# Kernel optimization log

Hardware: AMD Instinct MI355X
Metric: run time of the kernel (lower is better)

## Reference

```python
import jax, jax.numpy as jnp
import numpy as np

N_NODES = 100000


def _gcn_norm(edge_index, num_nodes):
    """Replicates remove_self_loops + add_self_loops + symmetric deg norm.

    Instead of dynamically removing/appending edges (data-dependent shapes),
    we mask out self-loop edges and handle the added self loops analytically:
    each node gets exactly one self loop with value deg_inv_sqrt[i]**2.
    """
    row, col = edge_index[0], edge_index[1]
    not_self = (row != col).astype(jnp.float32)  # mask removed self loops
    # degree(row) after removing self loops and adding one self loop per node
    deg = jax.ops.segment_sum(not_self, row, num_segments=num_nodes) + 1.0
    deg_inv_sqrt = jnp.where(deg > 0, jax.lax.rsqrt(deg), 0.0)
    edge_norm = deg_inv_sqrt[row] * deg_inv_sqrt[col] * not_self  # [E]
    self_norm = deg_inv_sqrt * deg_inv_sqrt  # [N] diagonal of normalized adj
    return row, col, edge_norm, self_norm


def _spmm(row, col, edge_norm, self_norm, h):
    # y = A_norm @ h, with A_norm = off-diagonal edges + diagonal self loops
    msgs = edge_norm[:, None] * h[col]  # [E, F] gather + scale
    y = jax.ops.segment_sum(msgs, row, num_segments=h.shape[0])
    return y + self_norm[:, None] * h


def setup_inputs() -> dict:
    key = jax.random.key(0)
    k1, k2, k3 = jax.random.split(key, 3)
    E = 3200000
    edge_index = jax.random.randint(k1, (2, E), 0, N_NODES, dtype=jnp.int32)
    x = jax.random.normal(k2, (N_NODES, 128), dtype=jnp.float32)
    W = jax.random.normal(k3, (128, 64), dtype=jnp.float32)
    return {"edge_index": edge_index, "x": x, "W": W}


def reference(edge_index, x, W):
    num_nodes = x.shape[0]
    row, col, edge_norm, self_norm = _gcn_norm(edge_index, num_nodes)
    h = x @ W  # [N, out]
    # matmul(A@A, h) == A @ (A @ h): avoid materializing sparse A^2
    h = _spmm(row, col, edge_norm, self_norm, h)
    h = _spmm(row, col, edge_norm, self_norm, h)
    return h
```

## Files before the change

### kernel.cpp

```cpp
#include <hip/hip_runtime.h>
#include <hip/hip_fp16.h>


#define RPB 1024
#define RPB_SHIFT 10
#define CBITS 17
#define CMASK ((1 << CBITS) - 1)
#define P1_TPB 1024
#define P1_EPT 8
#define P1_CHUNK (P1_TPB * P1_EPT)
#define MAXNB 128
#define BCAP 36864

typedef _Float16 f16x8 __attribute__((ext_vector_type(8)));
typedef float f32x4 __attribute__((ext_vector_type(4)));

__global__ __launch_bounds__(128) void k_init_bcur(int* __restrict__ bcur, int nb) {
  int b = blockIdx.x * 128 + threadIdx.x;
  if (b < nb) bcur[b] = b * BCAP;
}

__global__ __launch_bounds__(P1_TPB) void k_part1(const int* __restrict__ rows,
                                                  const int* __restrict__ cols,
                                                  int* __restrict__ bcur,
                                                  int* __restrict__ pairs,
                                                  int E, int nb) {
  __shared__ int hist[MAXNB];
  __shared__ int goff[MAXNB];
  int tid = threadIdx.x;
  long base = (long)blockIdx.x * P1_CHUNK;
  int r[P1_EPT], c[P1_EPT];
#pragma unroll
  for (int i = 0; i < P1_EPT; ++i) {
    long e = base + (long)i * P1_TPB + tid;
    if (e < E) {
      r[i] = rows[e];
      c[i] = cols[e];
    } else {
      r[i] = -1;
      c[i] = -1;
    }
  }
  if (tid < nb) hist[tid] = 0;
  __syncthreads();
#pragma unroll
  for (int i = 0; i < P1_EPT; ++i)
    if (r[i] != c[i]) atomicAdd(&hist[r[i] >> RPB_SHIFT], 1);
  __syncthreads();
  if (tid < nb) {
    int h = hist[tid];
    goff[tid] = h ? atomicAdd(&bcur[tid], h) : 0;
    hist[tid] = 0;
  }
  __syncthreads();
#pragma unroll
  for (int i = 0; i < P1_EPT; ++i) {
    if (r[i] != c[i]) {
      int b = r[i] >> RPB_SHIFT;
      int rank = atomicAdd(&hist[b], 1);
      pairs[goff[b] + rank] = ((r[i] & (RPB - 1)) << CBITS) | c[i];
    }
  }
}

__global__ __launch_bounds__(P1_TPB) void k_part3(const int* __restrict__ bcur,
                                                  const int* __restrict__ pairs,
                                                  int* __restrict__ colidx,
                                                  int* __restrict__ row_start,
                                                  int* __restrict__ deg,
                                                  float* __restrict__ dis,
                                                  float* __restrict__ selfn, int n) {
  __shared__ int lh[RPB];
  __shared__ int lscan[RPB];
  int tid = threadIdx.x;
  int b = blockIdx.x;
  int base = b * RPB;
  int e0 = b * BCAP;
  int e1 = bcur[b];
  lh[tid] = 0;
  __syncthreads();
  for (int i = e0 + tid; i < e1; i += P1_TPB)
    atomicAdd(&lh[pairs[i] >> CBITS], 1);
  __syncthreads();
  int d = lh[tid];
  int row = base + tid;
  if (row < n) {
    float dd = (float)d + 1.0f;
    dis[row] = rsqrtf(dd);
    selfn[row] = 1.0f / dd;
    deg[row] = d;
  }
  lscan[tid] = d;
  __syncthreads();
  for (int off = 1; off < RPB; off <<= 1) {
    int t = (tid >= off) ? lscan[tid - off] : 0;
    __syncthreads();
    lscan[tid] += t;
    __syncthreads();
  }
  int rstart = e0 + lscan[tid] - d;
  if (row < n) row_start[row] = rstart;
  lh[tid] = rstart;
  __syncthreads();
  for (int i = e0 + tid; i < e1; i += P1_TPB) {
    int v = pairs[i];
    int p = atomicAdd(&lh[v >> CBITS], 1);
    colidx[p] = v & CMASK;
  }
}

#define XPAD 136
__global__ __launch_bounds__(256) void k_gemm_mfma(const float* __restrict__ x,
                                                   const float* __restrict__ W,
                                                   const float* __restrict__ dis,
                                                   __half* __restrict__ g, int n) {
  __shared__ _Float16 xs[64 * XPAD];
  __shared__ _Float16 wt[64 * XPAD];
  int tid = threadIdx.x;
  int row0 = blockIdx.x * 64;
  for (int i = 0; i < 32; ++i) {
    int idx = tid + i * 256;
    int k = idx >> 6, f = idx & 63;
    wt[f * XPAD + k] = (_Float16)W[idx];
  }
  {
    int lrow = tid >> 2;
    int kb = (tid & 3) * 32;
    int row = row0 + lrow;
    _Float16* dst = &xs[lrow * XPAD + kb];
    if (row < n) {
      const float* src = x + (size_t)row * 128 + kb;
#pragma unroll
      for (int jj = 0; jj < 4; ++jj) {
        float4 v0 = *(const float4*)(src + jj * 8);
        float4 v1 = *(const float4*)(src + jj * 8 + 4);
        f16x8 t;
        t[0] = (_Float16)v0.x; t[1] = (_Float16)v0.y;
        t[2] = (_Float16)v0.z; t[3] = (_Float16)v0.w;
        t[4] = (_Float16)v1.x; t[5] = (_Float16)v1.y;
        t[6] = (_Float16)v1.z; t[7] = (_Float16)v1.w;
        *(f16x8*)(dst + jj * 8) = t;
      }
    } else {
      f16x8 z = {};
#pragma unroll
      for (int jj = 0; jj < 4; ++jj) *(f16x8*)(dst + jj * 8) = z;
    }
  }
  __syncthreads();
  int wid = tid >> 6, lane = tid & 63;
  int lr = lane & 15;
  int lk = (lane >> 4) * 8;
  f32x4 acc[4] = {{0.f, 0.f, 0.f, 0.f}, {0.f, 0.f, 0.f, 0.f},
                  {0.f, 0.f, 0.f, 0.f}, {0.f, 0.f, 0.f, 0.f}};
  const _Float16* xbase = &xs[(wid * 16 + lr) * XPAD + lk];
  const _Float16* wbase = &wt[lr * XPAD + lk];
#pragma unroll
  for (int ks = 0; ks < 4; ++ks) {
    f16x8 a = *(const f16x8*)(xbase + ks * 32);
#pragma unroll
    for (int ft = 0; ft < 4; ++ft) {
      f16x8 b = *(const f16x8*)(wbase + (size_t)ft * 16 * XPAD + ks * 32);
      acc[ft] = __builtin_amdgcn_mfma_f32_16x16x32_f16(a, b, acc[ft], 0, 0, 0);
    }
  }
  int mrow = row0 + wid * 16 + (lane >> 4) * 4;
#pragma unroll
  for (int j = 0; j < 4; ++j) {
    int row = mrow + j;
    if (row < n) {
      float dsc = dis[row];
#pragma unroll
      for (int ft = 0; ft < 4; ++ft)
        g[(size_t)row * 64 + ft * 16 + lr] = __float2half_rn(dsc * acc[ft][j]);
    }
  }
}

template <bool OUTF32>
__global__ __launch_bounds__(256) void k_spmm_h(const int* __restrict__ row_start,
                                                const int* __restrict__ deg,
                                                const int* __restrict__ colidx,
                                                const float* __restrict__ scale,
                                                const __half* __restrict__ gin,
                                                void* __restrict__ gout, int n) {
  int lane = threadIdx.x & 63;
  int wid = threadIdx.x >> 6;
  int r = blockIdx.x * 8 + wid * 2 + (lane >> 5);
  if (r >= n) return;
  int f2 = lane & 31;
  const __half2* gin2 = (const __half2*)gin;
  int start = row_start[r];
  int len = deg[r];
  float2 sv = __half22float2(gin2[(size_t)r * 32 + f2]);
  float ax = sv.x, ay = sv.y;
  int j = 0;
  for (; j + 16 <= len; j += 16) {
    int c[16];
#pragma unroll
    for (int u = 0; u < 16; ++u) c[u] = colidx[start + j + u];
    float2 v[16];
#pragma unroll
    for (int u = 0; u < 16; ++u) v[u] = __half22float2(gin2[(size_t)c[u] * 32 + f2]);
#pragma unroll
    for (int u = 0; u < 16; ++u) {
      ax += v[u].x;
      ay += v[u].y;
    }
  }
  for (; j + 4 <= len; j += 4) {
    int c0 = colidx[start + j + 0];
    int c1 = colidx[start + j + 1];
    int c2 = colidx[start + j + 2];
    int c3 = colidx[start + j + 3];
    float2 v0 = __half22float2(gin2[(size_t)c0 * 32 + f2]);
    float2 v1 = __half22float2(gin2[(size_t)c1 * 32 + f2]);
    float2 v2 = __half22float2(gin2[(size_t)c2 * 32 + f2]);
    float2 v3 = __half22float2(gin2[(size_t)c3 * 32 + f2]);
    ax += v0.x + v1.x + v2.x + v3.x;
    ay += v0.y + v1.y + v2.y + v3.y;
  }
  for (; j < len; ++j) {
    int c = colidx[start + j];
    float2 v = __half22float2(gin2[(size_t)c * 32 + f2]);
    ax += v.x;
    ay += v.y;
  }
  float s = scale[r];
  if (OUTF32) {
    ((float2*)gout)[(size_t)r * 32 + f2] = make_float2(s * ax, s * ay);
  } else {
    ((__half2*)gout)[(size_t)r * 32 + f2] = __floats2half2_rn(s * ax, s * ay);
  }
}

extern "C" void kernel_launch(void* const* d_in, const int* in_sizes, int n_in,
                              void* d_out, int out_size, void* d_ws, size_t ws_size,
                              hipStream_t stream) {
  const int* edge = (const int*)d_in[0];
  const float* x = (const float*)d_in[1];
  const float* W = (const float*)d_in[2];
  float* out = (float*)d_out;

  int E = in_sizes[0] / 2;
  int N = in_sizes[1] / 128;
  const int* rows = edge;
  const int* cols = edge + E;
  int nbuckets = (N + RPB - 1) / RPB;

  char* p = (char*)d_ws;
  auto alloc = [&](size_t bytes) {
    char* q = p;
    p += (bytes + 255) & ~(size_t)255;
    return q;
  };
  size_t slots = (size_t)nbuckets * BCAP;
  int* deg       = (int*)alloc((size_t)N * 4);
  int* row_start = (int*)alloc((size_t)N * 4);
  int* bcur      = (int*)alloc((size_t)nbuckets * 4);
  int* colidx    = (int*)alloc(slots * 4);
  float* dis     = (float*)alloc((size_t)N * 4);
  float* selfn   = (float*)alloc((size_t)N * 4);
  __half* g      = (__half*)alloc((size_t)N * 64 * 2);
  size_t g1_bytes = (size_t)N * 64 * 2;
  size_t pairs_bytes = slots * 4;
  char* g1_raw = (char*)alloc(g1_bytes > pairs_bytes ? g1_bytes : pairs_bytes);
  __half* g1 = (__half*)g1_raw;
  int* pairs = (int*)g1_raw;

  int p1_blocks = (int)(((long)E + P1_CHUNK - 1) / P1_CHUNK);

  k_init_bcur<<<(nbuckets + 127) / 128, 128, 0, stream>>>(bcur, nbuckets);
  k_part1<<<p1_blocks, P1_TPB, 0, stream>>>(rows, cols, bcur, pairs, E, nbuckets);
  k_part3<<<nbuckets, P1_TPB, 0, stream>>>(bcur, pairs, colidx, row_start, deg,
                                           dis, selfn, N);

  k_gemm_mfma<<<(N + 63) / 64, 256, 0, stream>>>(x, W, dis, g, N);

  k_spmm_h<false><<<(N + 7) / 8, 256, 0, stream>>>(row_start, deg, colidx, selfn,
                                                   g, (void*)g1, N);

  k_spmm_h<true><<<(N + 7) / 8, 256, 0, stream>>>(row_start, deg, colidx, dis,
                                                  g1, (void*)out, N);
}
```

Before: 194.7 us.

## Split feature dimension into 16-wide slices to shrink SpMM gather working set

The GEMM now writes the fp16 features in a sliced layout of four slices, each [N,16]. Each SpMM pass is split into four launches that process one 16-feature slice, so the gathered table per launch is N*32 bytes and fits better in cache, with 8 lanes per row instead of 32. Column-index loads and output stores are marked nontemporal so they do not evict the gather table. The cost is reading colidx four times per pass, issuing eight SpMM launches instead of two, and doing 32-byte gathers per neighbor.

```diff
diff --git a/kernel.cpp b/kernel.cpp
--- a/kernel.cpp
+++ b/kernel.cpp
@@ -14,6 +14,7 @@
 
 typedef _Float16 f16x8 __attribute__((ext_vector_type(8)));
 typedef float f32x4 __attribute__((ext_vector_type(4)));
+typedef float f32x2 __attribute__((ext_vector_type(2)));
 
 __global__ __launch_bounds__(128) void k_init_bcur(int* __restrict__ bcur, int nb) {
   int b = blockIdx.x * 128 + threadIdx.x;
@@ -172,36 +173,39 @@
       float dsc = dis[row];
 #pragma unroll
       for (int ft = 0; ft < 4; ++ft)
-        g[(size_t)row * 64 + ft * 16 + lr] = __float2half_rn(dsc * acc[ft][j]);
+        g[((size_t)ft * n + row) * 16 + lr] = __float2half_rn(dsc * acc[ft][j]);
     }
   }
 }
 
 template <bool OUTF32>
-__global__ __launch_bounds__(256) void k_spmm_h(const int* __restrict__ row_start,
+__global__ __launch_bounds__(256) void k_spmm_s(const int* __restrict__ row_start,
                                                 const int* __restrict__ deg,
                                                 const int* __restrict__ colidx,
                                                 const float* __restrict__ scale,
-                                                const __half* __restrict__ gin,
-                                                void* __restrict__ gout, int n) {
-  int lane = threadIdx.x & 63;
-  int wid = threadIdx.x >> 6;
-  int r = blockIdx.x * 8 + wid * 2 + (lane >> 5);
+                                                const __half2* __restrict__ gslice,
+                                                void* __restrict__ gout,
+                                                int n, int fbase) {
+  int tid = threadIdx.x;
+  int lane = tid & 63;
+  int wid = tid >> 6;
+  int rslot = lane >> 3;
+  int f2 = lane & 7;
+  int r = blockIdx.x * 32 + wid * 8 + rslot;
   if (r >= n) return;
-  int f2 = lane & 31;
-  const __half2* gin2 = (const __half2*)gin;
   int start = row_start[r];
   int len = deg[r];
-  float2 sv = __half22float2(gin2[(size_t)r * 32 + f2]);
+  float2 sv = __half22float2(gslice[r * 8 + f2]);
   float ax = sv.x, ay = sv.y;
   int j = 0;
   for (; j + 16 <= len; j += 16) {
     int c[16];
 #pragma unroll
-    for (int u = 0; u < 16; ++u) c[u] = colidx[start + j + u];
+    for (int u = 0; u < 16; ++u)
+      c[u] = __builtin_nontemporal_load(&colidx[start + j + u]);
     float2 v[16];
 #pragma unroll
-    for (int u = 0; u < 16; ++u) v[u] = __half22float2(gin2[(size_t)c[u] * 32 + f2]);
+    for (int u = 0; u < 16; ++u) v[u] = __half22float2(gslice[c[u] * 8 + f2]);
 #pragma unroll
     for (int u = 0; u < 16; ++u) {
       ax += v[u].x;
@@ -209,28 +213,33 @@
     }
   }
   for (; j + 4 <= len; j += 4) {
-    int c0 = colidx[start + j + 0];
-    int c1 = colidx[start + j + 1];
-    int c2 = colidx[start + j + 2];
-    int c3 = colidx[start + j + 3];
-    float2 v0 = __half22float2(gin2[(size_t)c0 * 32 + f2]);
-    float2 v1 = __half22float2(gin2[(size_t)c1 * 32 + f2]);
-    float2 v2 = __half22float2(gin2[(size_t)c2 * 32 + f2]);
-    float2 v3 = __half22float2(gin2[(size_t)c3 * 32 + f2]);
+    int c0 = __builtin_nontemporal_load(&colidx[start + j + 0]);
+    int c1 = __builtin_nontemporal_load(&colidx[start + j + 1]);
+    int c2 = __builtin_nontemporal_load(&colidx[start + j + 2]);
+    int c3 = __builtin_nontemporal_load(&colidx[start + j + 3]);
+    float2 v0 = __half22float2(gslice[c0 * 8 + f2]);
+    float2 v1 = __half22float2(gslice[c1 * 8 + f2]);
+    float2 v2 = __half22float2(gslice[c2 * 8 + f2]);
+    float2 v3 = __half22float2(gslice[c3 * 8 + f2]);
     ax += v0.x + v1.x + v2.x + v3.x;
     ay += v0.y + v1.y + v2.y + v3.y;
   }
   for (; j < len; ++j) {
-    int c = colidx[start + j];
-    float2 v = __half22float2(gin2[(size_t)c * 32 + f2]);
+    int c = __builtin_nontemporal_load(&colidx[start + j]);
+    float2 v = __half22float2(gslice[c * 8 + f2]);
     ax += v.x;
     ay += v.y;
   }
   float s = scale[r];
   if (OUTF32) {
-    ((float2*)gout)[(size_t)r * 32 + f2] = make_float2(s * ax, s * ay);
+    f32x2 val = {s * ax, s * ay};
+    f32x2* op = (f32x2*)((float*)gout + (size_t)r * 64 + fbase + f2 * 2);
+    __builtin_nontemporal_store(val, op);
   } else {
-    ((__half2*)gout)[(size_t)r * 32 + f2] = __floats2half2_rn(s * ax, s * ay);
+    __half2 hv = __floats2half2_rn(s * ax, s * ay);
+    unsigned int bits;
+    __builtin_memcpy(&bits, &hv, 4);
+    __builtin_nontemporal_store(bits, (unsigned int*)gout + (size_t)r * 8 + f2);
   }
 }
 
@@ -269,6 +278,7 @@
   int* pairs = (int*)g1_raw;
 
   int p1_blocks = (int)(((long)E + P1_CHUNK - 1) / P1_CHUNK);
+  int sp_blocks = (N + 31) / 32;
 
   k_init_bcur<<<(nbuckets + 127) / 128, 128, 0, stream>>>(bcur, nbuckets);
   k_part1<<<p1_blocks, P1_TPB, 0, stream>>>(rows, cols, bcur, pairs, E, nbuckets);
@@ -277,9 +287,17 @@
 
   k_gemm_mfma<<<(N + 63) / 64, 256, 0, stream>>>(x, W, dis, g, N);
 
-  k_spmm_h<false><<<(N + 7) / 8, 256, 0, stream>>>(row_start, deg, colidx, selfn,
-                                                   g, (void*)g1, N);
-
-  k_spmm_h<true><<<(N + 7) / 8, 256, 0, stream>>>(row_start, deg, colidx, dis,
-                                                  g1, (void*)out, N);
-}
+  for (int ps = 0; ps < 4; ++ps) {
+    k_spmm_s<false><<<sp_blocks, 256, 0, stream>>>(
+        row_start, deg, colidx, selfn,
+        (const __half2*)(g + (size_t)ps * N * 16),
+        (void*)(g1 + (size_t)ps * N * 16), N, ps * 16);
+  }
+
+  for (int ps = 0; ps < 4; ++ps) {
+    k_spmm_s<true><<<sp_blocks, 256, 0, stream>>>(
+        row_start, deg, colidx, dis,
+        (const __half2*)(g1 + (size_t)ps * N * 16),
+        (void*)out, N, ps * 16);
+  }
+}
```

After: 366.9 us. +88.4%, slower.
